# Performance work log

Measured on AMD Instinct MI355X. Metric: run time of the kernel, lower is better.

The kernel has to match this reference:

```python
import jax, jax.numpy as jnp
import numpy as np

N = 100000
E = 1600000
F_IN = 256
F_OUT = 128
ALPHA = 0.2  # leaky relu slope


def setup_inputs() -> dict:
    key = jax.random.key(0)
    ks = jax.random.split(key, 8)
    x = jax.random.normal(ks[0], (N, F_IN), dtype=jnp.float32)
    edge_index = jax.random.randint(ks[1], (2, E), 0, N, dtype=jnp.int64)
    edge_attr = jax.random.normal(ks[2], (E,), dtype=jnp.float32)
    # xavier-normal-ish params
    weight = jax.random.normal(ks[3], (F_IN, F_OUT), dtype=jnp.float32) * (1.414 * np.sqrt(2.0 / (F_IN + F_OUT)))
    bias = jnp.zeros((F_OUT,), dtype=jnp.float32)
    a_l = jax.random.normal(ks[4], (F_OUT,), dtype=jnp.float32) * 0.1
    a_r = jax.random.normal(ks[5], (F_OUT,), dtype=jnp.float32) * 0.1
    fc = jax.random.normal(ks[6], (F_OUT, 1), dtype=jnp.float32) * (1.414 * np.sqrt(2.0 / (F_OUT + 1)))
    bf = jnp.zeros((1,), dtype=jnp.float32)
    return {"x": x, "edge_index": edge_index, "edge_attr": edge_attr,
            "weight": weight, "bias": bias, "a_l": a_l, "a_r": a_r,
            "fc": fc, "bf": bf}


def _segment_softmax(val, seg, num_segments):
    # numerically stable softmax over edges grouped by destination row
    seg_max = jax.ops.segment_max(val, seg, num_segments=num_segments)
    val = jnp.exp(val - seg_max[seg])
    seg_sum = jax.ops.segment_sum(val, seg, num_segments=num_segments)
    return val / (seg_sum[seg] + 1e-16)


def reference(x, edge_index, edge_attr, weight, bias, a_l, a_r, fc, bf):
    # dropout layers are identity in eval mode (deterministic reference)
    h = x @ weight                                   # [N, F_OUT]
    row, col = edge_index[0], edge_index[1]          # dst, src
    # GAT-style edge attention: leaky_relu(a_l.h[dst] + a_r.h[src])
    score_l = h @ a_l                                # [N]
    score_r = h @ a_r                                # [N]
    e = score_l[row] + score_r[col]                  # [E]
    e = jnp.where(e > 0, e, ALPHA * e)
    # row-softmax normalization over incoming edges of each dst node
    val = _segment_softmax(e, row, N)                # [E]
    # spmm: out[i] = sum_{(i,j) in E} val_ij * h[j]
    val_h = jax.ops.segment_sum(val[:, None] * h[col], row, num_segments=N)  # [N, F_OUT]
    val_h = jnp.where(jnp.isnan(val_h), 0.0, val_h)
    val_h = val_h + bias
    # NodeAdaptiveEncoder: relu(x) + sigmoid(x@fc + bf) * min(x, 0)
    gate = jax.nn.sigmoid(val_h @ fc + bf)           # [N, 1]
    out = jnp.where(val_h < 0, 0.0, val_h) + gate * jnp.where(val_h > 0, 0.0, val_h)
    return out
```

## Files before the change

kernel.cpp:

```cpp
#include <hip/hip_runtime.h>

#define N_NODES 100000
#define N_EDGES 1600000
#define FIN 256
#define FOUT 128
#define LRELU_ALPHA 0.2f
#define LOG2E 1.4426950408889634f

#define NBUCKET 391
#define PBLOCKS 256
#define PCHUNK  (N_EDGES / PBLOCKS)
#define BCAP    5120

using bf16x8 = __attribute__((ext_vector_type(8))) short;
using f32x4  = __attribute__((ext_vector_type(4))) float;

static __device__ __forceinline__ unsigned short f2bf(float f) {
    union { float f; unsigned u; } v; v.f = f;
    unsigned r = (v.u + 0x7FFF + ((v.u >> 16) & 1)) >> 16;
    return (unsigned short)r;
}

static __device__ __forceinline__ bf16x8 cvt8(float4 a, float4 b) {
    union { bf16x8 v; unsigned short u[8]; } r;
    r.u[0] = f2bf(a.x); r.u[1] = f2bf(a.y); r.u[2] = f2bf(a.z); r.u[3] = f2bf(a.w);
    r.u[4] = f2bf(b.x); r.u[5] = f2bf(b.y); r.u[6] = f2bf(b.z); r.u[7] = f2bf(b.w);
    return r.v;
}

static __device__ __forceinline__ void gld_lds16(const unsigned short* g, unsigned short* l) {
    __builtin_amdgcn_global_load_lds(
        (const __attribute__((address_space(1))) unsigned int*)g,
        (__attribute__((address_space(3))) unsigned int*)l, 16, 0, 0);
}

static __device__ __forceinline__ void acc8(float* acc, uint4 r, float w) {
    union { uint4 u; _Float16 h[8]; } c; c.u = r;
#pragma unroll
    for (int k = 0; k < 8; ++k)
        acc[k] = fmaf((float)c.h[k], w, acc[k]);
}

static __device__ __forceinline__ float edgew(float sl, float sr) {
    float e = sl + sr;
    return exp2f(fmaf(fminf(e, 0.f), LRELU_ALPHA, fmaxf(e, 0.f)));
}

__global__ void k_wt(const float* __restrict__ w, unsigned short* __restrict__ wt_sw,
                     int* __restrict__ bcnt)
{
    if (blockIdx.x == 0)
        for (int z = threadIdx.x; z < NBUCKET; z += 256) bcnt[z] = 0;
    int i = blockIdx.x * blockDim.x + threadIdx.x;
    if (i >= FIN * FOUT) return;
    int k = i >> 7, n = i & 127;
    wt_sw[n * FIN + (((k >> 3) ^ (n & 7)) << 3) + (k & 7)] = f2bf(w[k * FOUT + n]);
}

__global__ __launch_bounds__(256, 2) void k_gemm3(
    const float* __restrict__ x, const unsigned short* __restrict__ wt_sw,
    const float* __restrict__ a_l, const float* __restrict__ a_r,
    unsigned short* __restrict__ hb, float* __restrict__ score_l,
    float* __restrict__ score_r)
{
    __shared__ unsigned short wlds[FOUT * FIN];

    const int tid  = threadIdx.x;
    const int lane = tid & 63;
    const int wid  = tid >> 6;
    const int m    = lane & 15;
    const int q    = lane >> 4;

    {
        const unsigned short* g = wt_sw + wid * 8192;
        unsigned short*       l = wlds  + wid * 8192;
#pragma unroll
        for (int i = 0; i < 16; ++i)
            gld_lds16(g + i * 512 + lane * 8, l + i * 512);
    }

    const int row0 = blockIdx.x * 128 + wid * 32;
    int r0 = row0 + m;       if (r0 > N_NODES - 1) r0 = N_NODES - 1;
    int r1 = row0 + 16 + m;  if (r1 > N_NODES - 1) r1 = N_NODES - 1;
    const float* xp0 = x + (long)r0 * FIN + q * 8;
    const float* xp1 = x + (long)r1 * FIN + q * 8;

    float4 xb[2][2][2];
    xb[0][0][0] = *(const float4*)(xp0);        xb[0][0][1] = *(const float4*)(xp0 + 4);
    xb[0][1][0] = *(const float4*)(xp1);        xb[0][1][1] = *(const float4*)(xp1 + 4);
    xb[1][0][0] = *(const float4*)(xp0 + 32);   xb[1][0][1] = *(const float4*)(xp0 + 36);
    xb[1][1][0] = *(const float4*)(xp1 + 32);   xb[1][1][1] = *(const float4*)(xp1 + 36);

    f32x4 acc[2][8];
#pragma unroll
    for (int mt = 0; mt < 2; ++mt)
#pragma unroll
        for (int nt = 0; nt < 8; ++nt) acc[mt][nt] = (f32x4){0.f, 0.f, 0.f, 0.f};

    __syncthreads();

    const int xr = m & 7;

    bf16x8 bfr[2][8];
#pragma unroll
    for (int nt = 0; nt < 8; ++nt)
        bfr[0][nt] = *(const bf16x8*)&wlds[(nt * 16 + m) * FIN + ((q ^ xr) << 3)];

#pragma unroll
    for (int s = 0; s < 8; ++s) {
        const int p = s & 1;
        bf16x8 a0 = cvt8(xb[p][0][0], xb[p][0][1]);
        bf16x8 a1 = cvt8(xb[p][1][0], xb[p][1][1]);
        if (s + 2 < 8) {
            xb[p][0][0] = *(const float4*)(xp0 + (s + 2) * 32);
            xb[p][0][1] = *(const float4*)(xp0 + (s + 2) * 32 + 4);
            xb[p][1][0] = *(const float4*)(xp1 + (s + 2) * 32);
            xb[p][1][1] = *(const float4*)(xp1 + (s + 2) * 32 + 4);
        }
        if (s + 1 < 8) {
#pragma unroll
            for (int nt = 0; nt < 8; ++nt)
                bfr[1 - p][nt] = *(const bf16x8*)
                    &wlds[(nt * 16 + m) * FIN + ((((s + 1) * 4 + q) ^ xr) << 3)];
        }
#pragma unroll
        for (int nt = 0; nt < 8; ++nt) {
            acc[0][nt] = __builtin_amdgcn_mfma_f32_16x16x32_bf16(bfr[p][nt], a0, acc[0][nt], 0, 0, 0);
            acc[1][nt] = __builtin_amdgcn_mfma_f32_16x16x32_bf16(bfr[p][nt], a1, acc[1][nt], 0, 0, 0);
        }
    }

    _Float16* hh = (_Float16*)hb;

#pragma unroll
    for (int mt = 0; mt < 2; ++mt) {
        const int node = row0 + mt * 16 + m;
        const bool ok = node < N_NODES;
        float sl = 0.f, sr = 0.f;
#pragma unroll
        for (int nt = 0; nt < 8; ++nt) {
            float4 alv = *(const float4*)(a_l + nt * 16 + q * 4);
            float4 arv = *(const float4*)(a_r + nt * 16 + q * 4);
            union { _Float16 h[4]; uint2 u; } pk;
#pragma unroll
            for (int r = 0; r < 4; ++r) {
                float v = acc[mt][nt][r];
                pk.h[r] = (_Float16)v;
                sl = fmaf(v, (&alv.x)[r], sl);
                sr = fmaf(v, (&arv.x)[r], sr);
            }
            if (ok) *(uint2*)&hh[node * FOUT + nt * 16 + q * 4] = pk.u;
        }
        sl += __shfl_xor(sl, 16, 64); sl += __shfl_xor(sl, 32, 64);
        sr += __shfl_xor(sr, 16, 64); sr += __shfl_xor(sr, 32, 64);
        if (ok && q == 0) {
            score_l[node] = sl * LOG2E;
            score_r[node] = sr * LOG2E;
        }
    }
}

__global__ __launch_bounds__(512) void k_part(const int* __restrict__ ei,
                                              int* __restrict__ bcnt,
                                              unsigned* __restrict__ part)
{
    __shared__ unsigned staging[PCHUNK];
    __shared__ unsigned short bkt[PCHUNK];
    __shared__ int cnt[512];
    __shared__ int loc[512];
    __shared__ int gbase[NBUCKET];

    const int tid = threadIdx.x;
    const int e0  = blockIdx.x * PCHUNK;

    cnt[tid] = 0;
    __syncthreads();

    for (int i = tid; i < PCHUNK; i += 512)
        atomicAdd(&cnt[ei[e0 + i] >> 8], 1);
    __syncthreads();

    int v = cnt[tid];
    loc[tid] = v;
    __syncthreads();
    for (int off = 1; off < 512; off <<= 1) {
        int t = (tid >= off) ? loc[tid - off] : 0;
        __syncthreads();
        loc[tid] += t;
        __syncthreads();
    }
    int excl = loc[tid] - v;
    if (tid < NBUCKET && v > 0) gbase[tid] = atomicAdd(&bcnt[tid], v);
    loc[tid] = excl;
    cnt[tid] = excl;
    __syncthreads();

    for (int i = tid; i < PCHUNK; i += 512) {
        int dst = ei[e0 + i];
        int src = ei[N_EDGES + e0 + i];
        int b = dst >> 8;
        unsigned rec = ((unsigned)(dst & 255) << 17) | (unsigned)src;
        int p = atomicAdd(&cnt[b], 1);
        staging[p] = rec;
        bkt[p] = (unsigned short)b;
    }
    __syncthreads();

    for (int i = tid; i < PCHUNK; i += 512) {
        int b = bkt[i];
        int off = gbase[b] + (i - loc[b]);
        if (off < BCAP) part[b * BCAP + off] = staging[i];
    }
}

__global__ __launch_bounds__(512) void k_bucket(const unsigned* __restrict__ part,
                                                const int* __restrict__ bcnt,
                                                int* __restrict__ rowbeg,
                                                int* __restrict__ rowend,
                                                unsigned* __restrict__ csrs)
{
    __shared__ unsigned rin[BCAP];
    __shared__ unsigned rs[BCAP];
    __shared__ int hist[256];
    __shared__ int tmp[512];

    const int b   = blockIdx.x;
    const int tid = threadIdx.x;
    const int beg = b * BCAP;
    int cnt = bcnt[b];
    if (cnt > BCAP) cnt = BCAP;
    const int d0 = b << 8;

    if (tid < 256) hist[tid] = 0;
    __syncthreads();

    for (int i = tid; i < cnt; i += 512) {
        unsigned rec = part[beg + i];
        rin[i] = rec;
        atomicAdd(&hist[rec >> 17], 1);
    }
    __syncthreads();

    int v = (tid < 256) ? hist[tid] : 0;
    tmp[tid] = v;
    __syncthreads();
    for (int off = 1; off < 512; off <<= 1) {
        int t = (tid >= off) ? tmp[tid - off] : 0;
        __syncthreads();
        tmp[tid] += t;
        __syncthreads();
    }
    if (tid < 256) {
        int excl = tmp[tid] - v;
        hist[tid] = excl;
        int d = d0 + tid;
        if (d < N_NODES) { rowbeg[d] = beg + excl; rowend[d] = beg + excl + v; }
    }
    __syncthreads();

    for (int i = tid; i < cnt; i += 512) {
        unsigned rec = rin[i];
        int p = atomicAdd(&hist[rec >> 17], 1);
        rs[p] = rec;
    }
    __syncthreads();

    for (int i = tid; i < cnt; i += 512)
        csrs[beg + i] = rs[i];
}

__global__ __launch_bounds__(256) void k_spmm_gate(
    const int* __restrict__ rowbeg, const int* __restrict__ rowend,
    const unsigned* __restrict__ csrs,
    const unsigned short* __restrict__ hb,
    const float* __restrict__ score_l, const float* __restrict__ score_r,
    const float* __restrict__ bias, const float* __restrict__ fc,
    const float* __restrict__ bf, float* __restrict__ out, int node0)
{
    const int lane = threadIdx.x & 63;
    const int g    = lane >> 4;
    const int t    = lane & 15;
    const int node = node0 + blockIdx.x * 4 + (threadIdx.x >> 6);
    if (node >= N_NODES) return;

    const int beg = rowbeg[node], end = rowend[node];
    const float sl = score_l[node];
    const unsigned short* __restrict__ hq = hb + (t << 3);

    float acc[8] = {0.f, 0.f, 0.f, 0.f, 0.f, 0.f, 0.f, 0.f};
    float denom = 0.f;

    if (end > beg) {
        const int nit  = (end - beg + 3) >> 2;
        const int nv   = nit - 1;
        const int last = end - 1;
        int j = beg + g;

        unsigned rec1;
        float sr0; uint4 r0;
        {
            unsigned rec0 = csrs[min(j, last)];
            rec1 = csrs[min(j + 4, last)];
            int s0 = rec0 & 0x1FFFF;
            sr0 = score_r[s0];
            r0  = *(const uint4*)(hq + (s0 << 7));
        }

        int i = 0;
        for (; i + 2 <= nv; i += 2) {
            unsigned rec2 = csrs[min(j + 8, last)];
            int s1 = rec1 & 0x1FFFF;
            float sr1 = score_r[s1];
            uint4 r1  = *(const uint4*)(hq + (s1 << 7));
            float w0 = edgew(sl, sr0);
            denom += w0;
            acc8(acc, r0, w0);
            j += 4;
            unsigned rec3 = csrs[min(j + 8, last)];
            int s2 = rec2 & 0x1FFFF;
            float sr2 = score_r[s2];
            uint4 r2  = *(const uint4*)(hq + (s2 << 7));
            float w1 = edgew(sl, sr1);
            denom += w1;
            acc8(acc, r1, w1);
            j += 4;
            rec1 = rec3; sr0 = sr2; r0 = r2;
        }
        if (i < nv) {
            int s1 = rec1 & 0x1FFFF;
            float sr1 = score_r[s1];
            uint4 r1  = *(const uint4*)(hq + (s1 << 7));
            float w0 = edgew(sl, sr0);
            denom += w0;
            acc8(acc, r0, w0);
            j += 4;
            sr0 = sr1; r0 = r1;
        }
        {
            float w = (j < end) ? edgew(sl, sr0) : 0.f;
            denom += w;
            acc8(acc, r0, w);
        }
    }

#pragma unroll
    for (int k = 0; k < 8; ++k) {
        acc[k] += __shfl_xor(acc[k], 16, 64);
        acc[k] += __shfl_xor(acc[k], 32, 64);
    }
    denom += __shfl_xor(denom, 16, 64);
    denom += __shfl_xor(denom, 32, 64);

    const float inv = 1.0f / (denom + 1e-16f);

    float vx[8];
    float gp = 0.f;
#pragma unroll
    for (int i = 0; i < 8; ++i) {
        vx[i] = fmaf(acc[i], inv, bias[t * 8 + i]);
        gp = fmaf(vx[i], fc[t * 8 + i], gp);
    }
#pragma unroll
    for (int msk = 1; msk < 16; msk <<= 1) gp += __shfl_xor(gp, msk, 64);
    const float gate = 1.0f / (1.0f + __expf(-(gp + bf[0])));

    float4 o;
    float* ov = &o.x;
    if (g == 0) {
#pragma unroll
        for (int i = 0; i < 4; ++i) {
            float v2 = vx[i];
            ov[i] = (v2 < 0.f ? 0.f : v2) + gate * (v2 > 0.f ? 0.f : v2);
        }
        *(float4*)&out[node * FOUT + t * 8] = o;
    } else if (g == 1) {
#pragma unroll
        for (int i = 0; i < 4; ++i) {
            float v2 = vx[4 + i];
            ov[i] = (v2 < 0.f ? 0.f : v2) + gate * (v2 > 0.f ? 0.f : v2);
        }
        *(float4*)&out[node * FOUT + t * 8 + 4] = o;
    }
}

extern "C" void kernel_launch(void* const* d_in, const int* in_sizes, int n_in,
                              void* d_out, int out_size, void* d_ws, size_t ws_size,
                              hipStream_t stream)
{
    const float* x      = (const float*)d_in[0];
    const int*   ei     = (const int*)d_in[1];
    const float* weight = (const float*)d_in[3];
    const float* bias   = (const float*)d_in[4];
    const float* a_l    = (const float*)d_in[5];
    const float* a_r    = (const float*)d_in[6];
    const float* fc     = (const float*)d_in[7];
    const float* bf     = (const float*)d_in[8];
    float* out = (float*)d_out;

    char* ws = (char*)d_ws;
    unsigned short* hb      = (unsigned short*)(ws);
    unsigned short* wt_sw   = (unsigned short*)(ws + 25600000);
    float*          score_l = (float*)(ws + 25665536);
    float*          score_r = (float*)(ws + 26065536);
    int*            bcnt    = (int*)  (ws + 26465536);
    int*            rowbeg  = (int*)  (ws + 26467584);
    int*            rowend  = (int*)  (ws + 26867584);
    unsigned*       part    = (unsigned*)(ws + 27267584);
    unsigned*       csrs    = (unsigned*)(ws + 35275264);

    k_wt<<<(FIN * FOUT + 255) / 256, 256, 0, stream>>>(weight, wt_sw, bcnt);

    k_gemm3<<<(N_NODES + 127) / 128, 256, 0, stream>>>(
        x, wt_sw, a_l, a_r, hb, score_l, score_r);

    k_part<<<PBLOCKS, 512, 0, stream>>>(ei, bcnt, part);
    k_bucket<<<NBUCKET, 512, 0, stream>>>(part, bcnt, rowbeg, rowend, csrs);

    k_spmm_gate<<<12500, 256, 0, stream>>>(
        rowbeg, rowend, csrs, hb, score_l, score_r, bias, fc, bf, out, 0);
    k_spmm_gate<<<12500, 256, 0, stream>>>(
        rowbeg, rowend, csrs, hb, score_l, score_r, bias, fc, bf, out, 50000);
}
```

Measured before the change: 296.9 us.

## Halve GEMM weight LDS footprint, double partition blocks, merge SpMM launches

The GEMM kernel now stages the bf16 weight matrix through LDS in two K-halves of 32 KB each instead of one 64 KB copy. This lets launch bounds target 3 blocks per CU, at the cost of an extra reload with two barriers mid-loop and losing the register double-buffering of B fragments. Separately, the edge partition kernel uses twice as many blocks, and the two half-range SpMM launches are merged into a single launch to cut launch overhead.

New measurement: 296.8 us. About the same (-0.0%).

```diff
diff --git a/kernel.cpp b/kernel.cpp
--- a/kernel.cpp
+++ b/kernel.cpp
@@ -8,7 +8,7 @@
 #define LOG2E 1.4426950408889634f
 
 #define NBUCKET 391
-#define PBLOCKS 256
+#define PBLOCKS 512
 #define PCHUNK  (N_EDGES / PBLOCKS)
 #define BCAP    5120
 
@@ -57,13 +57,13 @@
     wt_sw[n * FIN + (((k >> 3) ^ (n & 7)) << 3) + (k & 7)] = f2bf(w[k * FOUT + n]);
 }
 
-__global__ __launch_bounds__(256, 2) void k_gemm3(
+__global__ __launch_bounds__(256, 3) void k_gemm3(
     const float* __restrict__ x, const unsigned short* __restrict__ wt_sw,
     const float* __restrict__ a_l, const float* __restrict__ a_r,
     unsigned short* __restrict__ hb, float* __restrict__ score_l,
     float* __restrict__ score_r)
 {
-    __shared__ unsigned short wlds[FOUT * FIN];
+    __shared__ unsigned short wlds[FOUT * FIN / 2];
 
     const int tid  = threadIdx.x;
     const int lane = tid & 63;
@@ -72,11 +72,13 @@
     const int q    = lane >> 4;
 
     {
-        const unsigned short* g = wt_sw + wid * 8192;
-        unsigned short*       l = wlds  + wid * 8192;
-#pragma unroll
-        for (int i = 0; i < 16; ++i)
-            gld_lds16(g + i * 512 + lane * 8, l + i * 512);
+        const int cb = wid * 512;
+#pragma unroll
+        for (int i = 0; i < 8; ++i) {
+            int c = cb + i * 64 + lane;
+            gld_lds16(wt_sw + ((c >> 4) << 8) + ((c & 15) << 3),
+                      wlds + ((cb + i * 64) << 3));
+        }
     }
 
     const int row0 = blockIdx.x * 128 + wid * 32;
@@ -100,11 +102,6 @@
     __syncthreads();
 
     const int xr = m & 7;
-
-    bf16x8 bfr[2][8];
-#pragma unroll
-    for (int nt = 0; nt < 8; ++nt)
-        bfr[0][nt] = *(const bf16x8*)&wlds[(nt * 16 + m) * FIN + ((q ^ xr) << 3)];
 
 #pragma unroll
     for (int s = 0; s < 8; ++s) {
@@ -117,16 +114,26 @@
             xb[p][1][0] = *(const float4*)(xp1 + (s + 2) * 32);
             xb[p][1][1] = *(const float4*)(xp1 + (s + 2) * 32 + 4);
         }
-        if (s + 1 < 8) {
-#pragma unroll
-            for (int nt = 0; nt < 8; ++nt)
-                bfr[1 - p][nt] = *(const bf16x8*)
-                    &wlds[(nt * 16 + m) * FIN + ((((s + 1) * 4 + q) ^ xr) << 3)];
-        }
+        if (s == 4) {
+            __syncthreads();
+            const int cb = wid * 512;
+#pragma unroll
+            for (int i = 0; i < 8; ++i) {
+                int c = cb + i * 64 + lane;
+                gld_lds16(wt_sw + ((c >> 4) << 8) + 128 + ((c & 15) << 3),
+                          wlds + ((cb + i * 64) << 3));
+            }
+            __syncthreads();
+        }
+        bf16x8 bfr[8];
+#pragma unroll
+        for (int nt = 0; nt < 8; ++nt)
+            bfr[nt] = *(const bf16x8*)
+                &wlds[(nt * 16 + m) * 128 + (((((s & 3) * 4) + q) ^ xr) << 3)];
 #pragma unroll
         for (int nt = 0; nt < 8; ++nt) {
-            acc[0][nt] = __builtin_amdgcn_mfma_f32_16x16x32_bf16(bfr[p][nt], a0, acc[0][nt], 0, 0, 0);
-            acc[1][nt] = __builtin_amdgcn_mfma_f32_16x16x32_bf16(bfr[p][nt], a1, acc[1][nt], 0, 0, 0);
+            acc[0][nt] = __builtin_amdgcn_mfma_f32_16x16x32_bf16(bfr[nt], a0, acc[0][nt], 0, 0, 0);
+            acc[1][nt] = __builtin_amdgcn_mfma_f32_16x16x32_bf16(bfr[nt], a1, acc[1][nt], 0, 0, 0);
         }
     }
 
@@ -275,12 +282,12 @@
     const unsigned short* __restrict__ hb,
     const float* __restrict__ score_l, const float* __restrict__ score_r,
     const float* __restrict__ bias, const float* __restrict__ fc,
-    const float* __restrict__ bf, float* __restrict__ out, int node0)
+    const float* __restrict__ bf, float* __restrict__ out)
 {
     const int lane = threadIdx.x & 63;
     const int g    = lane >> 4;
     const int t    = lane & 15;
-    const int node = node0 + blockIdx.x * 4 + (threadIdx.x >> 6);
+    const int node = blockIdx.x * 4 + (threadIdx.x >> 6);
     if (node >= N_NODES) return;
 
     const int beg = rowbeg[node], end = rowend[node];
@@ -416,8 +423,6 @@
     k_part<<<PBLOCKS, 512, 0, stream>>>(ei, bcnt, part);
     k_bucket<<<NBUCKET, 512, 0, stream>>>(part, bcnt, rowbeg, rowend, csrs);
 
-    k_spmm_gate<<<12500, 256, 0, stream>>>(
-        rowbeg, rowend, csrs, hb, score_l, score_r, bias, fc, bf, out, 0);
-    k_spmm_gate<<<12500, 256, 0, stream>>>(
-        rowbeg, rowend, csrs, hb, score_l, score_r, bias, fc, bf, out, 50000);
-}
+    k_spmm_gate<<<(N_NODES + 3) / 4, 256, 0, stream>>>(
+        rowbeg, rowend, csrs, hb, score_l, score_r, bias, fc, bf, out);
+}
```
